# Kernel optimization log

Measured on AMD Instinct MI355X. Metric: run time of the kernel, lower is better.

## Reference

```python
import jax, jax.numpy as jnp
import numpy as np

P = 64       # number of pathways
NV = 512     # features per pathway (nvar[i])
W = 256      # hidden width per pathway
COV = 16     # covariates
B = 2048     # batch
EPS = 1e-5   # BatchNorm eps
SLOPE = 0.2  # LeakyReLU negative slope


def _lrelu(v):
    return jnp.where(v >= 0, v, SLOPE * v)


def setup_inputs() -> dict:
    key = jax.random.key(0)
    ks = jax.random.split(key, 8)
    x = jax.random.normal(ks[0], (B, P * NV + COV), dtype=jnp.float32)
    # per-pathway weights (no bias), stacked across pathways -> grouped GEMM
    W1 = jax.random.normal(ks[1], (P, NV, W), dtype=jnp.float32) * (1.0 / np.sqrt(NV))
    W2 = jax.random.normal(ks[2], (P, W, W), dtype=jnp.float32) * (1.0 / np.sqrt(W))
    W3 = jax.random.normal(ks[3], (P, W), dtype=jnp.float32) * (1.0 / np.sqrt(W))
    gamma = jnp.ones((P,), dtype=jnp.float32)   # bn_path weight
    beta = jnp.zeros((P,), dtype=jnp.float32)   # bn_path bias
    fc_w = jax.random.normal(ks[4], (P + COV, 1), dtype=jnp.float32) * 0.05
    fc_b = jnp.full((1,), 0.001, dtype=jnp.float32)
    return {"x": x, "W1": W1, "W2": W2, "W3": W3,
            "gamma": gamma, "beta": beta, "fc_w": fc_w, "fc_b": fc_b}


def reference(x, W1, W2, W3, gamma, beta, fc_w, fc_b):
    # pathway blocks (dropout = identity in eval): grouped GEMMs over P pathways
    xp = x[:, : P * NV].reshape(B, P, NV)
    h = _lrelu(jnp.einsum('bpi,pio->bpo', xp, W1))
    h = _lrelu(jnp.einsum('bpi,pio->bpo', h, W2))
    p = _lrelu(jnp.einsum('bpi,pi->bp', h, W3))          # [B, P]
    # BatchNorm1d (training-mode batch statistics, biased variance)
    mean = p.mean(axis=0)
    var = p.var(axis=0)
    pn = (p - mean) / jnp.sqrt(var + EPS) * gamma + beta
    # global L2 (Frobenius) normalization, as torch.norm(pathway_layer, 2)
    pn = pn / jnp.linalg.norm(pn)
    # concat covariates, final linear + sigmoid
    z = jnp.concatenate([pn, x[:, P * NV: P * NV + COV]], axis=1)  # [B, P+COV]
    return jax.nn.sigmoid(z @ fc_w + fc_b)                         # [B, 1]
```

## Files before the change

kernel.cpp:

```cpp
#include <hip/hip_runtime.h>
#include <hip/hip_bf16.h>

#define PW 64
#define NV 512
#define HW 256
#define COV 16
#define BATCH 2048
#define XROW (PW * NV + COV)
#define IMG 16384
#define IMG2 8192

typedef short s16x8 __attribute__((ext_vector_type(8)));
typedef float f32x4 __attribute__((ext_vector_type(4)));

__device__ __forceinline__ unsigned short f2bf(float f) {
    union { float f; unsigned int u; } v;
    v.f = f;
    unsigned int u = v.u;
    unsigned int r = (u + 0x7fffu + ((u >> 16) & 1u)) >> 16;
    return (unsigned short)r;
}

__device__ __forceinline__ unsigned int pack2(float a, float b) {
    __hip_bfloat162 h = __float22bfloat162_rn(float2{a, b});
    union { __hip_bfloat162 h; unsigned int u; } c;
    c.h = h;
    return c.u;
}

__device__ __forceinline__ float lrelu(float v) { return v >= 0.f ? v : 0.2f * v; }

__device__ __forceinline__ void gl_lds16(const void* g, void* l) {
    __builtin_amdgcn_global_load_lds(
        (const __attribute__((address_space(1))) void*)g,
        (__attribute__((address_space(3))) void*)l, 16, 0, 0);
}

__global__ __launch_bounds__(256)
void transpose_all(const float* __restrict__ W1, const float* __restrict__ W2,
                   unsigned short* __restrict__ W1I, unsigned short* __restrict__ W2I) {
    __shared__ float tile[64][260];
    int bx = blockIdx.x;
    const int t = threadIdx.x;
    const bool isW1 = bx < 512;
    const float* src;
    if (isW1) {
        int p = bx >> 3, kb = bx & 7;
        src = W1 + ((size_t)p * NV + kb * 64) * HW;
    } else {
        int b2 = bx - 512;
        int p = b2 >> 2, kb64 = b2 & 3;
        src = W2 + ((size_t)p * HW + kb64 * 64) * HW;
    }
    #pragma unroll
    for (int i = 0; i < 16; ++i) {
        int idx = t + i * 256;
        int r = idx >> 6, c4 = (idx & 63) << 2;
        *(float4*)&tile[r][c4] = *(const float4*)(src + (size_t)r * HW + c4);
    }
    __syncthreads();
    if (isW1) {
        int p = bx >> 3, kb = bx & 7;
        unsigned short* dst = W1I + (size_t)(p * 8 + kb) * IMG;
        #pragma unroll
        for (int pass = 0; pass < 8; ++pass) {
            int idx = pass * 256 + t;
            int n = idx >> 3, s = idx & 7;
            int g = s ^ (n & 7);
            unsigned short v[8];
            #pragma unroll
            for (int j = 0; j < 8; ++j)
                v[j] = f2bf(tile[g * 8 + j][n]);
            *(s16x8*)(dst + (size_t)idx * 8) = *(s16x8*)v;
        }
    } else {
        int b2 = bx - 512;
        int p = b2 >> 2, kb64 = b2 & 3;
        unsigned short* dst = W2I + (size_t)(p * 8 + kb64 * 2) * IMG2;
        #pragma unroll
        for (int pass = 0; pass < 8; ++pass) {
            int idx = pass * 256 + t;
            int h = idx >> 10;
            int rem = idx & 1023;
            int n = rem >> 2, s = rem & 3;
            int g = s ^ ((n >> 1) & 3);
            int krow = h * 32 + g * 8;
            unsigned short v[8];
            #pragma unroll
            for (int j = 0; j < 8; ++j)
                v[j] = f2bf(tile[krow + j][n]);
            *(s16x8*)(dst + (size_t)h * IMG2 + n * 32 + s * 8) = *(s16x8*)v;
        }
    }
}

__global__ __launch_bounds__(256, 2)
void pathway_fused(const float* __restrict__ x, const unsigned short* __restrict__ W1I,
                   const unsigned short* __restrict__ W2I, const float* __restrict__ W3,
                   float* __restrict__ pvec) {
    __shared__ __align__(16) unsigned short lds[40960];

    const int lin = blockIdx.x;
    const int xcd = lin & 7;
    const int idx = lin >> 3;
    const int p   = xcd * 8 + (idx >> 5);
    const int m   = idx & 31;
    const int bm0 = m * 64;

    const int t = threadIdx.x;
    const int lane = t & 63;
    const int wave = t >> 6;
    const int wn   = wave * 64;
    const int l15  = lane & 15;
    const int quad = lane >> 4;

    const float* Ap          = x   + (size_t)p * NV;
    const unsigned short* B1 = W1I + (size_t)p * 8 * IMG;
    const unsigned short* B2 = W2I + (size_t)p * 8 * IMG2;

    int arow[4], acol[4], aoff[4];
    #pragma unroll
    for (int i = 0; i < 4; ++i) {
        int ii = t + i * 256;
        arow[i] = ii >> 4;
        acol[i] = (ii & 15) * 4;
        int slot = (acol[i] >> 3) ^ (arow[i] & 7);
        aoff[i] = arow[i] * 64 + slot * 8 + (acol[i] & 7);
    }

    float4 S0[4], S1[4];
    f32x4 acc[4][4] = {};

#define XLOAD(dst, k0) { \
    _Pragma("unroll") \
    for (int i = 0; i < 4; ++i) \
        dst[i] = *(const float4*)(Ap + (size_t)(bm0 + arow[i]) * XROW + (k0) + acol[i]); }

#define APACK(src, buf) { \
    unsigned short* Asb = lds + 32768 + (buf) * 4096; \
    _Pragma("unroll") \
    for (int i = 0; i < 4; ++i) { \
        uint2 u; \
        u.x = pack2(src[i].x, src[i].y); \
        u.y = pack2(src[i].z, src[i].w); \
        *(uint2*)&Asb[aoff[i]] = u; } }

#define B1STAGE(buf, kb) { \
    const unsigned short* img = B1 + (size_t)(kb) * IMG; \
    _Pragma("unroll") \
    for (int c = 0; c < 8; ++c) { \
        int off = wave * 8192 + c * 1024; \
        gl_lds16((const char*)img + off + lane * 16, (char*)lds + (buf) * 32768 + off); } }

#define MFMA_A(buf) { \
    const unsigned short* Asb = lds + 32768 + (buf) * 4096; \
    const unsigned short* Bsb = lds + (buf) * 16384; \
    __builtin_amdgcn_s_setprio(1); \
    _Pragma("unroll") \
    for (int kk = 0; kk < 64; kk += 32) { \
        s16x8 af[4], bfr[4]; \
        _Pragma("unroll") \
        for (int mi = 0; mi < 4; ++mi) { \
            int row = mi * 16 + l15; \
            int slot = ((kk >> 3) + quad) ^ (row & 7); \
            af[mi] = *(const s16x8*)&Asb[row * 64 + slot * 8]; } \
        _Pragma("unroll") \
        for (int ni = 0; ni < 4; ++ni) { \
            int row = wn + ni * 16 + l15; \
            int slot = ((kk >> 3) + quad) ^ (row & 7); \
            bfr[ni] = *(const s16x8*)&Bsb[row * 64 + slot * 8]; } \
        _Pragma("unroll") \
        for (int mi = 0; mi < 4; ++mi) \
            _Pragma("unroll") \
            for (int ni = 0; ni < 4; ++ni) \
                acc[mi][ni] = __builtin_amdgcn_mfma_f32_16x16x32_bf16( \
                    af[mi], bfr[ni], acc[mi][ni], 0, 0, 0); } \
    __builtin_amdgcn_s_setprio(0); }

#define W2STAGE(buf, kb) { \
    const unsigned short* img = B2 + (size_t)(kb) * IMG2; \
    _Pragma("unroll") \
    for (int c = 0; c < 4; ++c) { \
        int off = wave * 4096 + c * 1024; \
        gl_lds16((const char*)img + off + lane * 16, (char*)lds + 32768 + (buf) * 16384 + off); } }

#define MFMA_B(buf, kb) { \
    const unsigned short* W2b = lds + 16384 + (buf) * 8192; \
    __builtin_amdgcn_s_setprio(1); \
    { \
        s16x8 af[4], bfr[4]; \
        _Pragma("unroll") \
        for (int mi = 0; mi < 4; ++mi) { \
            int row = mi * 16 + l15; \
            int slot = ((kb) * 4 + quad) ^ (row & 7); \
            af[mi] = *(const s16x8*)&lds[row * 256 + slot * 8]; } \
        _Pragma("unroll") \
        for (int ni = 0; ni < 4; ++ni) { \
            int row = wn + ni * 16 + l15; \
            int slot = quad ^ ((row >> 1) & 3); \
            bfr[ni] = *(const s16x8*)&W2b[row * 32 + slot * 8]; } \
        _Pragma("unroll") \
        for (int mi = 0; mi < 4; ++mi) \
            _Pragma("unroll") \
            for (int ni = 0; ni < 4; ++ni) \
                acc[mi][ni] = __builtin_amdgcn_mfma_f32_16x16x32_bf16( \
                    af[mi], bfr[ni], acc[mi][ni], 0, 0, 0); \
    } \
    __builtin_amdgcn_s_setprio(0); }

    XLOAD(S0, 0);
    B1STAGE(0, 0);
    APACK(S0, 0);
    XLOAD(S0, 64);
    __syncthreads();

    #pragma unroll
    for (int s2 = 0; s2 < 4; ++s2) {
        const int te = 2 * s2;
        if (te + 1 < 8) B1STAGE(1, te + 1);
        if (te + 1 < 8) APACK(S0, 1);
        if (te + 2 < 8) XLOAD(S1, (te + 2) * 64);
        MFMA_A(0);
        __syncthreads();
        const int to = te + 1;
        if (to + 1 < 8) B1STAGE(0, to + 1);
        if (to + 1 < 8) APACK(S1, 0);
        if (to + 2 < 8) XLOAD(S0, (to + 2) * 64);
        MFMA_A(1);
        __syncthreads();
    }

    #pragma unroll
    for (int mi = 0; mi < 4; ++mi)
        #pragma unroll
        for (int ni = 0; ni < 4; ++ni)
            #pragma unroll
            for (int r = 0; r < 4; ++r) {
                int row = mi * 16 + quad * 4 + r;
                int col = wn + ni * 16 + l15;
                int slot = (col >> 3) ^ (row & 7);
                lds[row * 256 + slot * 8 + (col & 7)] = f2bf(lrelu(acc[mi][ni][r]));
            }
    W2STAGE(0, 0);
    __syncthreads();

    #pragma unroll
    for (int mi = 0; mi < 4; ++mi)
        #pragma unroll
        for (int ni = 0; ni < 4; ++ni)
            acc[mi][ni] = (f32x4){0.f, 0.f, 0.f, 0.f};

    #pragma unroll
    for (int s2 = 0; s2 < 4; ++s2) {
        const int te = 2 * s2;
        if (te + 1 < 8) W2STAGE(1, te + 1);
        MFMA_B(0, te);
        __syncthreads();
        const int to = te + 1;
        if (to + 1 < 8) W2STAGE(0, to + 1);
        MFMA_B(1, to);
        __syncthreads();
    }

    float* red = (float*)(lds + 32768);
    float w3v[4];
    #pragma unroll
    for (int ni = 0; ni < 4; ++ni)
        w3v[ni] = W3[(size_t)p * HW + wn + ni * 16 + l15];
    float part[4][4];
    #pragma unroll
    for (int mi = 0; mi < 4; ++mi) {
        #pragma unroll
        for (int r = 0; r < 4; ++r) {
            float s = 0.f;
            #pragma unroll
            for (int ni = 0; ni < 4; ++ni)
                s += lrelu(acc[mi][ni][r]) * w3v[ni];
            part[mi][r] = s;
        }
    }
    #pragma unroll
    for (int off = 1; off < 16; off <<= 1)
        #pragma unroll
        for (int mi = 0; mi < 4; ++mi)
            #pragma unroll
            for (int r = 0; r < 4; ++r)
                part[mi][r] += __shfl_xor(part[mi][r], off);
    if (l15 == 0)
        #pragma unroll
        for (int mi = 0; mi < 4; ++mi)
            #pragma unroll
            for (int r = 0; r < 4; ++r)
                red[wave * 64 + mi * 16 + quad * 4 + r] = part[mi][r];
    __syncthreads();
    if (t < 64) {
        float s = red[0 * 64 + t] + red[1 * 64 + t] + red[2 * 64 + t] + red[3 * 64 + t];
        pvec[(size_t)p * BATCH + bm0 + t] = lrelu(s);
    }
#undef XLOAD
#undef APACK
#undef B1STAGE
#undef MFMA_A
#undef W2STAGE
#undef MFMA_B
}

__global__ __launch_bounds__(256)
void stats_k(const float* __restrict__ pvec, float* __restrict__ stat) {
    const int p = blockIdx.x;
    float s = 0.f, q = 0.f;
    for (int i = threadIdx.x; i < BATCH; i += 256) {
        float v = pvec[(size_t)p * BATCH + i];
        s += v; q += v * v;
    }
    #pragma unroll
    for (int off = 32; off; off >>= 1) {
        s += __shfl_down(s, off);
        q += __shfl_down(q, off);
    }
    __shared__ float ls[4], lq[4];
    const int wave = threadIdx.x >> 6, lane = threadIdx.x & 63;
    if (lane == 0) { ls[wave] = s; lq[wave] = q; }
    __syncthreads();
    if (threadIdx.x == 0) {
        float S = ls[0] + ls[1] + ls[2] + ls[3];
        float Q = lq[0] + lq[1] + lq[2] + lq[3];
        float mean = S * (1.f / BATCH);
        float var  = Q * (1.f / BATCH) - mean * mean;
        stat[p]       = mean;
        stat[64 + p]  = rsqrtf(var + 1e-5f);
        stat[128 + p] = var;
    }
}

__global__ __launch_bounds__(256)
void final_k(const float* __restrict__ pvec, const float* __restrict__ stat,
             const float* __restrict__ gamma, const float* __restrict__ beta,
             const float* __restrict__ x, const float* __restrict__ fc_w,
             const float* __restrict__ fc_b, float* __restrict__ out) {
    const int b = blockIdx.x * 256 + threadIdx.x;
    float nsq = 0.f;
    #pragma unroll
    for (int p = 0; p < PW; ++p) {
        float g = gamma[p], bt = beta[p], var = stat[128 + p], inv = stat[64 + p];
        nsq += (float)BATCH * (g * g * var * inv * inv + bt * bt);
    }
    const float rn = rsqrtf(nsq);
    float acc = fc_b[0];
    #pragma unroll
    for (int p = 0; p < PW; ++p) {
        float pn = (pvec[(size_t)p * BATCH + b] - stat[p]) * stat[64 + p] * gamma[p] + beta[p];
        acc += pn * rn * fc_w[p];
    }
    #pragma unroll
    for (int c = 0; c < COV; ++c)
        acc += x[(size_t)b * XROW + PW * NV + c] * fc_w[PW + c];
    out[b] = 1.f / (1.f + __expf(-acc));
}

extern "C" void kernel_launch(void* const* d_in, const int* in_sizes, int n_in,
                              void* d_out, int out_size, void* d_ws, size_t ws_size,
                              hipStream_t stream) {
    const float* x     = (const float*)d_in[0];
    const float* W1    = (const float*)d_in[1];
    const float* W2    = (const float*)d_in[2];
    const float* W3    = (const float*)d_in[3];
    const float* gamma = (const float*)d_in[4];
    const float* beta  = (const float*)d_in[5];
    const float* fc_w  = (const float*)d_in[6];
    const float* fc_b  = (const float*)d_in[7];
    float* out = (float*)d_out;

    char* ws = (char*)d_ws;
    size_t off = 0;
    unsigned short* W1I = (unsigned short*)(ws + off); off += (size_t)PW * NV * HW * 2;
    unsigned short* W2I = (unsigned short*)(ws + off); off += (size_t)PW * HW * HW * 2;
    float* pvec = (float*)(ws + off); off += (size_t)PW * BATCH * 4;
    float* stat = (float*)(ws + off); off += 256 * 4;

    transpose_all<<<dim3(512 + 256), 256, 0, stream>>>(W1, W2, W1I, W2I);

    pathway_fused<<<dim3(2048), 256, 0, stream>>>(x, W1I, W2I, W3, pvec);

    stats_k<<<PW, 256, 0, stream>>>(pvec, stat);

    final_k<<<BATCH / 256, 256, 0, stream>>>(pvec, stat, gamma, beta, x, fc_w, fc_b, out);
}
```

Measured before the change: 488.1 us.

## Replace syncthreads with vmcnt-gated barriers and triple-buffer W2 staging

Replaces __syncthreads in the two GEMM phases with explicit s_waitcnt vmcnt(N) plus s_barrier, so newer prefetches can stay in flight across a barrier. The W2 phase moves to a three-slot ring with a two-step lookahead, and the first two W2 tiles are issued before the layer-1 activations are written to LDS. Scheduling barriers pin the order of loads, packing and MFMAs. The hand-counted vmcnt values must match the actual number of outstanding loads, or a race becomes possible. The W2 buffers also move to a different LDS region that must not overlap live data.

```diff
diff --git a/kernel.cpp b/kernel.cpp
--- a/kernel.cpp
+++ b/kernel.cpp
@@ -35,6 +35,10 @@
         (const __attribute__((address_space(1))) void*)g,
         (__attribute__((address_space(3))) void*)l, 16, 0, 0);
 }
+
+#define WAITV(n) asm volatile("s_waitcnt vmcnt(" #n ") lgkmcnt(0)" ::: "memory")
+#define BAR()    __builtin_amdgcn_s_barrier()
+#define SCHED0() __builtin_amdgcn_sched_barrier(0)
 
 __global__ __launch_bounds__(256)
 void transpose_all(const float* __restrict__ W1, const float* __restrict__ W2,
@@ -118,15 +122,18 @@
     const unsigned short* B1 = W1I + (size_t)p * 8 * IMG;
     const unsigned short* B2 = W2I + (size_t)p * 8 * IMG2;
 
-    int arow[4], acol[4], aoff[4];
+    int arow[4], aoff[4];
     #pragma unroll
     for (int i = 0; i < 4; ++i) {
         int ii = t + i * 256;
         arow[i] = ii >> 4;
-        acol[i] = (ii & 15) * 4;
-        int slot = (acol[i] >> 3) ^ (arow[i] & 7);
-        aoff[i] = arow[i] * 64 + slot * 8 + (acol[i] & 7);
-    }
+        int acol = (ii & 15) * 4;
+        int slot = (acol >> 3) ^ (arow[i] & 7);
+        aoff[i] = arow[i] * 64 + slot * 8 + (acol & 7);
+    }
+    int acolc[4];
+    #pragma unroll
+    for (int i = 0; i < 4; ++i) acolc[i] = ((t + i * 256) & 15) * 4;
 
     float4 S0[4], S1[4];
     f32x4 acc[4][4] = {};
@@ -134,7 +141,7 @@
 #define XLOAD(dst, k0) { \
     _Pragma("unroll") \
     for (int i = 0; i < 4; ++i) \
-        dst[i] = *(const float4*)(Ap + (size_t)(bm0 + arow[i]) * XROW + (k0) + acol[i]); }
+        dst[i] = *(const float4*)(Ap + (size_t)(bm0 + arow[i]) * XROW + (k0) + acolc[i]); }
 
 #define APACK(src, buf) { \
     unsigned short* Asb = lds + 32768 + (buf) * 4096; \
@@ -182,7 +189,7 @@
     _Pragma("unroll") \
     for (int c = 0; c < 4; ++c) { \
         int off = wave * 4096 + c * 1024; \
-        gl_lds16((const char*)img + off + lane * 16, (char*)lds + 32768 + (buf) * 16384 + off); } }
+        gl_lds16((const char*)img + off + lane * 16, (char*)lds + 16384 + (buf) * 8192 + off); } }
 
 #define MFMA_B(buf, kb) { \
     const unsigned short* W2b = lds + 16384 + (buf) * 8192; \
@@ -208,28 +215,46 @@
     } \
     __builtin_amdgcn_s_setprio(0); }
 
+#define STEP_A(tt, sLoad, sPack, WN) { \
+    if ((tt) + 1 < 8) B1STAGE(1 - ((tt) & 1), (tt) + 1); \
+    SCHED0(); \
+    if ((tt) + 2 < 8) XLOAD(sLoad, ((tt) + 2) * 64); \
+    if ((tt) + 1 < 8) APACK(sPack, 1 - ((tt) & 1)); \
+    MFMA_A((tt) & 1); \
+    WAITV(WN); \
+    BAR(); \
+    SCHED0(); }
+
+#define STEP_B(tt, WN) { \
+    if ((tt) + 2 < 8) W2STAGE(((tt) + 2) % 3, (tt) + 2); \
+    SCHED0(); \
+    MFMA_B((tt) % 3, (tt)); \
+    WAITV(WN); \
+    BAR(); \
+    SCHED0(); }
+
     XLOAD(S0, 0);
+    SCHED0();
     B1STAGE(0, 0);
+    SCHED0();
+    XLOAD(S1, 64);
     APACK(S0, 0);
-    XLOAD(S0, 64);
-    __syncthreads();
-
-    #pragma unroll
-    for (int s2 = 0; s2 < 4; ++s2) {
-        const int te = 2 * s2;
-        if (te + 1 < 8) B1STAGE(1, te + 1);
-        if (te + 1 < 8) APACK(S0, 1);
-        if (te + 2 < 8) XLOAD(S1, (te + 2) * 64);
-        MFMA_A(0);
-        __syncthreads();
-        const int to = te + 1;
-        if (to + 1 < 8) B1STAGE(0, to + 1);
-        if (to + 1 < 8) APACK(S1, 0);
-        if (to + 2 < 8) XLOAD(S0, (to + 2) * 64);
-        MFMA_A(1);
-        __syncthreads();
-    }
-
+    WAITV(4);
+    BAR();
+    SCHED0();
+
+    STEP_A(0, S0, S1, 4);
+    STEP_A(1, S1, S0, 4);
+    STEP_A(2, S0, S1, 4);
+    STEP_A(3, S1, S0, 4);
+    STEP_A(4, S0, S1, 4);
+    STEP_A(5, S1, S0, 4);
+    STEP_A(6, S0, S1, 0);
+    STEP_A(7, S1, S0, 0);
+
+    W2STAGE(0, 0);
+    SCHED0();
+    W2STAGE(1, 1);
     #pragma unroll
     for (int mi = 0; mi < 4; ++mi)
         #pragma unroll
@@ -241,8 +266,9 @@
                 int slot = (col >> 3) ^ (row & 7);
                 lds[row * 256 + slot * 8 + (col & 7)] = f2bf(lrelu(acc[mi][ni][r]));
             }
-    W2STAGE(0, 0);
-    __syncthreads();
+    WAITV(4);
+    BAR();
+    SCHED0();
 
     #pragma unroll
     for (int mi = 0; mi < 4; ++mi)
@@ -250,19 +276,16 @@
         for (int ni = 0; ni < 4; ++ni)
             acc[mi][ni] = (f32x4){0.f, 0.f, 0.f, 0.f};
 
-    #pragma unroll
-    for (int s2 = 0; s2 < 4; ++s2) {
-        const int te = 2 * s2;
-        if (te + 1 < 8) W2STAGE(1, te + 1);
-        MFMA_B(0, te);
-        __syncthreads();
-        const int to = te + 1;
-        if (to + 1 < 8) W2STAGE(0, to + 1);
-        MFMA_B(1, to);
-        __syncthreads();
-    }
-
-    float* red = (float*)(lds + 32768);
+    STEP_B(0, 4);
+    STEP_B(1, 4);
+    STEP_B(2, 4);
+    STEP_B(3, 4);
+    STEP_B(4, 4);
+    STEP_B(5, 4);
+    STEP_B(6, 0);
+    STEP_B(7, 0);
+
+    float* red = (float*)(lds + 16384);
     float w3v[4];
     #pragma unroll
     for (int ni = 0; ni < 4; ++ni)
@@ -303,6 +326,8 @@
 #undef MFMA_A
 #undef W2STAGE
 #undef MFMA_B
+#undef STEP_A
+#undef STEP_B
 }
 
 __global__ __launch_bounds__(256)
@@ -379,10 +404,7 @@
     float* stat = (float*)(ws + off); off += 256 * 4;
 
     transpose_all<<<dim3(512 + 256), 256, 0, stream>>>(W1, W2, W1I, W2I);
-
     pathway_fused<<<dim3(2048), 256, 0, stream>>>(x, W1I, W2I, W3, pvec);
-
     stats_k<<<PW, 256, 0, stream>>>(pvec, stat);
-
     final_k<<<BATCH / 256, 256, 0, stream>>>(pvec, stat, gamma, beta, x, fc_w, fc_b, out);
 }
```

Result: no change. 481.1 us (-1.4%).
